# Kernel tuning notes

Measured on AMD Instinct MI355X. Metric: run time of the kernel, lower is better.

Reference implementation:

```python
import jax, jax.numpy as jnp
import numpy as np

B, S, DIM, H, KVH = 2, 1024, 4096, 32, 8
HD = DIM // H          # 128
NREP = H // KVH        # 4
KVD = KVH * HD         # 1024
EPS = 1e-8


def setup_inputs() -> dict:
    key = jax.random.key(0)
    ks = jax.random.split(key, 6)
    x = jax.random.normal(ks[0], (B, S, DIM), jnp.float32)
    wq = jax.random.normal(ks[1], (DIM, DIM), jnp.float32) * 0.02
    wk = jax.random.normal(ks[2], (KVD, DIM), jnp.float32) * 0.02
    wv = jax.random.normal(ks[3], (KVD, DIM), jnp.float32) * 0.02
    wo = jax.random.normal(ks[4], (DIM, DIM), jnp.float32) * 0.02
    scale = jnp.ones((DIM,), jnp.float32)  # RMSNorm scale
    # freq_cis has shape (S, 1) complex so it broadcasts onto both the
    # (B,S,DIM/2) and (B,S,KVD/2) complex views (RoPE applied pre-head-split).
    theta = jnp.arange(S, dtype=jnp.float32)[:, None] * 0.01  # (S,1)
    freqs_cos = jnp.cos(theta)
    freqs_sin = jnp.sin(theta)
    return dict(x=x, scale=scale, wq=wq, wk=wk, wv=wv, wo=wo,
                freqs_cos=freqs_cos, freqs_sin=freqs_sin)


def _rope(t, cos, sin):
    # t: (B,S,D) viewed as (B,S,D/2,2) complex pairs; cos/sin: (S,1)
    t2 = t.reshape(*t.shape[:-1], -1, 2)
    t0, t1 = t2[..., 0], t2[..., 1]
    r0 = t0 * cos - t1 * sin
    r1 = t0 * sin + t1 * cos
    return jnp.stack([r0, r1], axis=-1).reshape(t.shape)


def reference(x, scale, wq, wk, wv, wo, freqs_cos, freqs_sin):
    # RMSNorm
    xn = scale * x * jax.lax.rsqrt(jnp.mean(x * x, axis=-1, keepdims=True) + EPS)
    # QKV projections (nn.Linear: y = x @ W^T)
    q = jnp.einsum('bsd,ed->bse', xn, wq)          # (B,S,DIM)
    k = jnp.einsum('bsd,ed->bse', xn, wk)          # (B,S,KVD)
    v = jnp.einsum('bsd,ed->bse', xn, wv)          # (B,S,KVD)
    # RoPE on full projected dims (as in the original, before head split)
    q = _rope(q, freqs_cos, freqs_sin)
    k = _rope(k, freqs_cos, freqs_sin)
    q = q.reshape(B, S, H, HD)
    k = k.reshape(B, S, KVH, HD)
    v = v.reshape(B, S, KVH, HD)
    # start_pos=0: KV-cache write then read of [:, :S] is identity.
    # GQA expansion via torch .repeat => tile along head axis
    k = jnp.tile(k, (1, 1, NREP, 1))               # (B,S,H,HD)
    v = jnp.tile(v, (1, 1, NREP, 1))
    logits = jnp.einsum('bqhd,bkhd->bhqk', q, k) / jnp.sqrt(jnp.float32(HD))
    causal = jnp.triu(jnp.ones((S, S), bool), 1)   # True above diagonal
    logits = jnp.where(causal, -jnp.inf, logits)
    attn = jax.nn.softmax(logits, axis=-1)
    out = jnp.einsum('bhqk,bkhd->bqhd', attn, v).reshape(B, S, DIM)
    # residual from the NORMALIZED x (the original rebinds x = norm(x))
    return xn + jnp.einsum('bsd,ed->bse', out, wo)
```

## Files before the change

kernel.cpp:

```cpp
#include <hip/hip_runtime.h>
#include <math.h>

#define NB    2
#define NS    1024
#define NDIM  4096
#define NH    32
#define NKVH  8
#define NHD   128
#define NKVD  1024
#define NM    (NB*NS)
#define NQKV  (NDIM + 2*NKVD)

typedef __attribute__((ext_vector_type(8))) short bf16x8;
typedef __attribute__((ext_vector_type(4))) float f32x4;

#define AS3(p) ((__attribute__((address_space(3))) void*)(p))
#define AS1(p) ((const __attribute__((address_space(1))) void*)(p))

__device__ __forceinline__ unsigned short f2bf(float f) {
  unsigned u = __builtin_bit_cast(unsigned, f);
  u += 0x7fffu + ((u >> 16) & 1u);
  return (unsigned short)(u >> 16);
}
__device__ __forceinline__ float bf2f(unsigned short h) {
  unsigned u = ((unsigned)h) << 16;
  return __builtin_bit_cast(float, u);
}
__device__ __forceinline__ void split2(float v, unsigned short& h, unsigned short& l) {
  h = f2bf(v);
  l = f2bf(v - bf2f(h));
}
__device__ __forceinline__ void split8(const float* f, bf16x8& h, bf16x8& l) {
#pragma unroll
  for (int i = 0; i < 8; ++i) {
    unsigned short hh, ll;
    split2(f[i], hh, ll);
    h[i] = (short)hh; l[i] = (short)ll;
  }
}

template <int OFMT>
__global__ __launch_bounds__(256) void rmsnorm_k(const float* __restrict__ x,
                                                 const float* __restrict__ scale,
                                                 unsigned short* __restrict__ xnh,
                                                 unsigned short* __restrict__ xnl,
                                                 float* __restrict__ xnf) {
  const int row = blockIdx.x;
  const float4* xr = (const float4*)(x + (size_t)row * NDIM);
  const float4* sc4 = (const float4*)scale;
  const int t = threadIdx.x;
  float4 v[4];
  float ss = 0.f;
#pragma unroll
  for (int i = 0; i < 4; ++i) {
    v[i] = xr[t + 256 * i];
    ss += v[i].x * v[i].x + v[i].y * v[i].y + v[i].z * v[i].z + v[i].w * v[i].w;
  }
#pragma unroll
  for (int m = 32; m >= 1; m >>= 1) ss += __shfl_xor(ss, m, 64);
  __shared__ float red[4];
  if ((t & 63) == 0) red[t >> 6] = ss;
  __syncthreads();
  const float r = rsqrtf((red[0] + red[1] + red[2] + red[3]) * (1.0f / NDIM) + 1e-8f);
#pragma unroll
  for (int i = 0; i < 4; ++i) {
    const float4 s4 = sc4[t + 256 * i];
    float o[4] = {v[i].x * r * s4.x, v[i].y * r * s4.y, v[i].z * r * s4.z, v[i].w * r * s4.w};
    if (OFMT == 0) {
      ushort4 h4, l4;
      split2(o[0], h4.x, l4.x); split2(o[1], h4.y, l4.y);
      split2(o[2], h4.z, l4.z); split2(o[3], h4.w, l4.w);
      *(ushort4*)&xnh[(size_t)row * NDIM + (t + 256 * i) * 4] = h4;
      *(ushort4*)&xnl[(size_t)row * NDIM + (t + 256 * i) * 4] = l4;
    } else {
      *(float4*)&xnf[(size_t)row * NDIM + (t + 256 * i) * 4] =
          make_float4(o[0], o[1], o[2], o[3]);
    }
  }
}

__global__ __launch_bounds__(256) void splitw_k(const float* __restrict__ src,
                                                unsigned short* __restrict__ dh,
                                                unsigned short* __restrict__ dl,
                                                long long count4) {
  const long long stride = (long long)gridDim.x * 256;
  for (long long i = blockIdx.x * 256LL + threadIdx.x; i < count4; i += stride) {
    const float4 v = ((const float4*)src)[i];
    ushort4 h4, l4;
    split2(v.x, h4.x, l4.x); split2(v.y, h4.y, l4.y);
    split2(v.z, h4.z, l4.z); split2(v.w, h4.w, l4.w);
    ((ushort4*)dh)[i] = h4;
    ((ushort4*)dl)[i] = l4;
  }
}

__global__ __launch_bounds__(256) void zerofill_k(float* __restrict__ p, long long n) {
  const long long stride = (long long)gridDim.x * 256;
  for (long long i = blockIdx.x * 256LL + threadIdx.x; i < n; i += stride) p[i] = 0.f;
}

template <int EPI>
__global__ __launch_bounds__(256) void gemm_split_k(
    const unsigned short* __restrict__ Ah, const unsigned short* __restrict__ Al,
    const unsigned short* __restrict__ Bh, const unsigned short* __restrict__ Bl,
    const float* __restrict__ fc, const float* __restrict__ fs,
    const unsigned short* __restrict__ resh, const unsigned short* __restrict__ resl,
    float* __restrict__ C, int ncol0) {
  constexpr int OW = (EPI == 0) ? NQKV : NDIM;
  __shared__ unsigned short lds[4][4096];

  const int t = threadIdx.x;
  const int wave = t >> 6, lane = t & 63;
  const int wr = wave >> 1, wc = wave & 1;
  const int m0 = blockIdx.x * 128;
  const int n0 = blockIdx.y * 128;

  const int srow = t >> 2;
  const int ke = (((t & 3) ^ ((srow >> 1) & 3)) * 8);
  const size_t arow0 = (size_t)(m0 + srow) * NDIM + ke;
  const size_t arow1 = (size_t)(m0 + 64 + srow) * NDIM + ke;
  const size_t brow0 = (size_t)(n0 + srow) * NDIM + ke;
  const size_t brow1 = (size_t)(n0 + 64 + srow) * NDIM + ke;
  const int ldsoff0 = wave * 512;
  const int ldsoff1 = 2048 + wave * 512;

  f32x4 acc[4][4];
#pragma unroll
  for (int i = 0; i < 4; ++i)
#pragma unroll
    for (int j = 0; j < 4; ++j) acc[i][j] = (f32x4){0.f, 0.f, 0.f, 0.f};

  const int fl = lane & 15;
  const int fq = lane >> 4;

  for (int k0 = 0; k0 < NDIM; k0 += 32) {
    __syncthreads();
    __builtin_amdgcn_global_load_lds(AS1(Ah + arow0 + k0), AS3(&lds[0][ldsoff0]), 16, 0, 0);
    __builtin_amdgcn_global_load_lds(AS1(Ah + arow1 + k0), AS3(&lds[0][ldsoff1]), 16, 0, 0);
    __builtin_amdgcn_global_load_lds(AS1(Al + arow0 + k0), AS3(&lds[1][ldsoff0]), 16, 0, 0);
    __builtin_amdgcn_global_load_lds(AS1(Al + arow1 + k0), AS3(&lds[1][ldsoff1]), 16, 0, 0);
    __builtin_amdgcn_global_load_lds(AS1(Bh + brow0 + k0), AS3(&lds[2][ldsoff0]), 16, 0, 0);
    __builtin_amdgcn_global_load_lds(AS1(Bh + brow1 + k0), AS3(&lds[2][ldsoff1]), 16, 0, 0);
    __builtin_amdgcn_global_load_lds(AS1(Bl + brow0 + k0), AS3(&lds[3][ldsoff0]), 16, 0, 0);
    __builtin_amdgcn_global_load_lds(AS1(Bl + brow1 + k0), AS3(&lds[3][ldsoff1]), 16, 0, 0);
    __syncthreads();

    bf16x8 fah[4], fal[4], fbh[4], fbl[4];
#pragma unroll
    for (int m = 0; m < 4; ++m) {
      const int r = wr * 64 + m * 16 + fl;
      const int idx = r * 32 + ((fq ^ ((r >> 1) & 3)) * 8);
      fah[m] = *(const bf16x8*)&lds[0][idx];
      fal[m] = *(const bf16x8*)&lds[1][idx];
    }
#pragma unroll
    for (int n = 0; n < 4; ++n) {
      const int r = wc * 64 + n * 16 + fl;
      const int idx = r * 32 + ((fq ^ ((r >> 1) & 3)) * 8);
      fbh[n] = *(const bf16x8*)&lds[2][idx];
      fbl[n] = *(const bf16x8*)&lds[3][idx];
    }
#pragma unroll
    for (int m = 0; m < 4; ++m)
#pragma unroll
      for (int n = 0; n < 4; ++n) {
        acc[m][n] = __builtin_amdgcn_mfma_f32_16x16x32_bf16(fah[m], fbh[n], acc[m][n], 0, 0, 0);
        acc[m][n] = __builtin_amdgcn_mfma_f32_16x16x32_bf16(fah[m], fbl[n], acc[m][n], 0, 0, 0);
        acc[m][n] = __builtin_amdgcn_mfma_f32_16x16x32_bf16(fal[m], fbh[n], acc[m][n], 0, 0, 0);
      }
  }

  if (EPI == 0) {
    const int nabs0 = ncol0 + n0;
    const bool rope = (nabs0 < NDIM + NKVD);
    const float qs = (nabs0 < NDIM) ? 0.08838834764831845f : 1.0f;
#pragma unroll
    for (int m = 0; m < 4; ++m)
#pragma unroll
      for (int j = 0; j < 4; ++j) {
        const int gm = m0 + wr * 64 + m * 16 + fq * 4 + j;
        const int si = gm & (NS - 1);
        const float c = fc[si], s = fs[si];
#pragma unroll
        for (int n = 0; n < 4; ++n) {
          const int gn = nabs0 + wc * 64 + n * 16 + fl;
          const float val = acc[m][n][j];
          float o;
          if (rope) {
            const float par = __shfl_xor(val, 1, 64);
            o = ((gn & 1) ? (val * c + par * s) : (val * c - par * s)) * qs;
          } else {
            o = val;
          }
          C[(size_t)gm * OW + gn] = o;
        }
      }
  } else {
#pragma unroll
    for (int m = 0; m < 4; ++m)
#pragma unroll
      for (int j = 0; j < 4; ++j) {
        const int gm = m0 + wr * 64 + m * 16 + fq * 4 + j;
#pragma unroll
        for (int n = 0; n < 4; ++n) {
          const int gn = n0 + wc * 64 + n * 16 + fl;
          const size_t ri = (size_t)gm * NDIM + gn;
          C[ri] = acc[m][n][j] + bf2f(resh[ri]) + bf2f(resl[ri]);
        }
      }
  }
}

__global__ __launch_bounds__(256) void attn_mfma_k(const float* __restrict__ qkv,
                                                   unsigned short* __restrict__ aoh,
                                                   unsigned short* __restrict__ aol) {
  const int qt = (NS / 64 - 1) - blockIdx.x;
  const int bh = blockIdx.y;
  const int b = bh >> 5;
  const int h = bh & 31;
  const int kvh = h & 7;
  const int q0 = qt * 64;

  __shared__ __align__(16) char ldsB[40960];

  const int t = threadIdx.x;
  const int w = t >> 6, lane = t & 63;
  const int l15 = lane & 15, lq = lane >> 4;

  bf16x8 qh[4], ql[4];
  {
    const float* qp = qkv + (size_t)(b * NS + q0 + w * 16 + l15) * NQKV + h * NHD;
#pragma unroll
    for (int c = 0; c < 4; ++c) {
      float qa[8];
      const float4 a = *(const float4*)(qp + lq * 8 + 32 * c);
      const float4 b2 = *(const float4*)(qp + lq * 8 + 32 * c + 4);
      qa[0] = a.x; qa[1] = a.y; qa[2] = a.z; qa[3] = a.w;
      qa[4] = b2.x; qa[5] = b2.y; qa[6] = b2.z; qa[7] = b2.w;
      split8(qa, qh[c], ql[c]);
    }
  }

  f32x4 o[8];
#pragma unroll
  for (int dt = 0; dt < 8; ++dt) o[dt] = (f32x4){0.f, 0.f, 0.f, 0.f};
  float m_run[4] = {-INFINITY, -INFINITY, -INFINITY, -INFINITY};
  float l_run[4] = {0.f, 0.f, 0.f, 0.f};

  const int ntiles = 2 * qt + 2;
  for (int jt = 0; jt < ntiles; ++jt) {
    const int kv0 = jt * 32;
    __syncthreads();
    {
      const int r = t >> 3, d0 = (t & 7) * 16;
      const float* kp = qkv + (size_t)(b * NS + kv0 + r) * NQKV + NDIM + kvh * NHD + d0;
      const float* vp = kp + NKVD;
      float kf[16], vf[16];
#pragma unroll
      for (int i = 0; i < 4; ++i) {
        const float4 k4 = *(const float4*)(kp + 4 * i);
        const float4 v4 = *(const float4*)(vp + 4 * i);
        kf[4 * i] = k4.x; kf[4 * i + 1] = k4.y; kf[4 * i + 2] = k4.z; kf[4 * i + 3] = k4.w;
        vf[4 * i] = v4.x; vf[4 * i + 1] = v4.y; vf[4 * i + 2] = v4.z; vf[4 * i + 3] = v4.w;
      }
#pragma unroll
      for (int g = 0; g < 2; ++g) {
        bf16x8 hi, lo;
        split8(kf + 8 * g, hi, lo);
        const int slotp = (((t & 7) * 2 + g) ^ (r & 7));
        *(bf16x8*)(ldsB + r * 256 + slotp * 16) = hi;
        *(bf16x8*)(ldsB + 8192 + r * 256 + slotp * 16) = lo;
      }
#pragma unroll
      for (int c = 0; c < 16; ++c) {
        const int d = d0 + c;
        unsigned short sh, sl;
        split2(vf[c], sh, sl);
        const int by = 16384 + d * 64 + (((r >> 3) ^ (d & 3)) * 16) + (r & 7) * 2;
        *(unsigned short*)(ldsB + by) = sh;
        *(unsigned short*)(ldsB + 8192 + by) = sl;
      }
    }
    __syncthreads();

    f32x4 s0 = (f32x4){0.f, 0.f, 0.f, 0.f}, s1 = (f32x4){0.f, 0.f, 0.f, 0.f};
    {
      const char* kb = ldsB + l15 * 256;
#pragma unroll
      for (int c = 0; c < 4; ++c) {
        const int sa = ((lq + 4 * c) ^ (l15 & 7)) * 16;
        const bf16x8 k0h = *(const bf16x8*)(kb + sa);
        const bf16x8 k0l = *(const bf16x8*)(kb + 8192 + sa);
        const bf16x8 k1h = *(const bf16x8*)(kb + 4096 + sa);
        const bf16x8 k1l = *(const bf16x8*)(kb + 12288 + sa);
        s0 = __builtin_amdgcn_mfma_f32_16x16x32_bf16(qh[c], k0h, s0, 0, 0, 0);
        s0 = __builtin_amdgcn_mfma_f32_16x16x32_bf16(qh[c], k0l, s0, 0, 0, 0);
        s0 = __builtin_amdgcn_mfma_f32_16x16x32_bf16(ql[c], k0h, s0, 0, 0, 0);
        s1 = __builtin_amdgcn_mfma_f32_16x16x32_bf16(qh[c], k1h, s1, 0, 0, 0);
        s1 = __builtin_amdgcn_mfma_f32_16x16x32_bf16(qh[c], k1l, s1, 0, 0, 0);
        s1 = __builtin_amdgcn_mfma_f32_16x16x32_bf16(ql[c], k1h, s1, 0, 0, 0);
      }
    }

    if (jt >= 2 * qt) {
#pragma unroll
      for (int j = 0; j < 4; ++j) {
        const int qg = q0 + w * 16 + lq * 4 + j;
        if (kv0 + l15 > qg) s0[j] = -INFINITY;
        if (kv0 + 16 + l15 > qg) s1[j] = -INFINITY;
      }
    }

    float resc[4];
#pragma unroll
    for (int j = 0; j < 4; ++j) {
      float mx = fmaxf(s0[j], s1[j]);
#pragma unroll
      for (int mm = 1; mm <= 8; mm <<= 1) mx = fmaxf(mx, __shfl_xor(mx, mm, 64));
      const float mn = fmaxf(m_run[j], mx);
      resc[j] = __expf(m_run[j] - mn);
      s0[j] = __expf(s0[j] - mn);
      s1[j] = __expf(s1[j] - mn);
      float ps = s0[j] + s1[j];
#pragma unroll
      for (int mm = 1; mm <= 8; mm <<= 1) ps += __shfl_xor(ps, mm, 64);
      l_run[j] = l_run[j] * resc[j] + ps;
      m_run[j] = mn;
    }
#pragma unroll
    for (int j = 0; j < 4; ++j) {
      const int q = w * 16 + lq * 4 + j;
      const int by0 = 32768 + q * 128 + (((l15 >> 2) ^ (q & 7)) * 16) + (l15 & 3) * 4;
      *(float*)(ldsB + by0) = s0[j];
      const int kv1 = 16 + l15;
      const int by1 = 32768 + q * 128 + (((kv1 >> 2) ^ (q & 7)) * 16) + (kv1 & 3) * 4;
      *(float*)(ldsB + by1) = s1[j];
    }
#pragma unroll
    for (int dt = 0; dt < 8; ++dt)
#pragma unroll
      for (int j = 0; j < 4; ++j) o[dt][j] *= resc[j];
    __syncthreads();

    {
      const int qrow = w * 16 + l15;
      const int byA = 32768 + qrow * 128 + (((2 * lq) ^ (qrow & 7)) * 16);
      const int byB = 32768 + qrow * 128 + (((2 * lq + 1) ^ (qrow & 7)) * 16);
      const float4 pA = *(const float4*)(ldsB + byA);
      const float4 pB = *(const float4*)(ldsB + byB);
      float pf[8] = {pA.x, pA.y, pA.z, pA.w, pB.x, pB.y, pB.z, pB.w};
      bf16x8 pah, pal;
      split8(pf, pah, pal);
#pragma unroll
      for (int dt = 0; dt < 8; ++dt) {
        const int vrow = dt * 16 + l15;
        const int bv = 16384 + vrow * 64 + ((lq ^ (vrow & 3)) * 16);
        const bf16x8 vbh = *(const bf16x8*)(ldsB + bv);
        const bf16x8 vbl = *(const bf16x8*)(ldsB + bv + 8192);
        o[dt] = __builtin_amdgcn_mfma_f32_16x16x32_bf16(pah, vbh, o[dt], 0, 0, 0);
        o[dt] = __builtin_amdgcn_mfma_f32_16x16x32_bf16(pah, vbl, o[dt], 0, 0, 0);
        o[dt] = __builtin_amdgcn_mfma_f32_16x16x32_bf16(pal, vbh, o[dt], 0, 0, 0);
      }
    }
  }

  float invl[4];
#pragma unroll
  for (int j = 0; j < 4; ++j) invl[j] = 1.0f / l_run[j];
#pragma unroll
  for (int j = 0; j < 4; ++j) {
    const size_t row = (size_t)(b * NS + q0 + w * 16 + lq * 4 + j) * NDIM + h * NHD;
#pragma unroll
    for (int dt = 0; dt < 8; ++dt) {
      unsigned short hh, ll;
      split2(o[dt][j] * invl[j], hh, ll);
      aoh[row + dt * 16 + l15] = hh;
      aol[row + dt * 16 + l15] = ll;
    }
  }
}

#define FBM 64
#define FBK 32
#define LPAD 68

template <int EPI>
__global__ __launch_bounds__(256) void gemm_f32_k(const float* __restrict__ A,
                                                  const float* __restrict__ Wq,
                                                  const float* __restrict__ Wk,
                                                  const float* __restrict__ Wv,
                                                  const float* __restrict__ fc,
                                                  const float* __restrict__ fs,
                                                  const float* __restrict__ resid,
                                                  float* __restrict__ C) {
  __shared__ float As[FBK][LPAD];
  __shared__ float Bs[FBK][LPAD];
  const int t = threadIdx.x;
  const int tx = t & 15, ty = t >> 4;
  const int m0 = blockIdx.y * FBM;
  const int n0 = blockIdx.x * FBM;

  const float* W;
  int wn0;
  if (EPI == 0) {
    if (n0 < NDIM)              { W = Wq; wn0 = n0; }
    else if (n0 < NDIM + NKVD)  { W = Wk; wn0 = n0 - NDIM; }
    else                        { W = Wv; wn0 = n0 - NDIM - NKVD; }
  } else {
    W = Wq; wn0 = n0;
  }

  const int srow = t >> 3;
  const int skk  = (t & 7) * 4;
  const float* Ar = A + (size_t)(m0 + srow) * NDIM + skk;
  const float* Br = W + (size_t)(wn0 + srow) * NDIM + skk;

  float acc[4][4] = {};

  for (int k0 = 0; k0 < NDIM; k0 += FBK) {
    const float4 a0 = *(const float4*)(Ar + k0);
    const float4 a1 = *(const float4*)(Ar + k0 + (size_t)32 * NDIM);
    const float4 b0 = *(const float4*)(Br + k0);
    const float4 b1 = *(const float4*)(Br + k0 + (size_t)32 * NDIM);
    __syncthreads();
    As[skk + 0][srow] = a0.x; As[skk + 1][srow] = a0.y;
    As[skk + 2][srow] = a0.z; As[skk + 3][srow] = a0.w;
    As[skk + 0][srow + 32] = a1.x; As[skk + 1][srow + 32] = a1.y;
    As[skk + 2][srow + 32] = a1.z; As[skk + 3][srow + 32] = a1.w;
    Bs[skk + 0][srow] = b0.x; Bs[skk + 1][srow] = b0.y;
    Bs[skk + 2][srow] = b0.z; Bs[skk + 3][srow] = b0.w;
    Bs[skk + 0][srow + 32] = b1.x; Bs[skk + 1][srow + 32] = b1.y;
    Bs[skk + 2][srow + 32] = b1.z; Bs[skk + 3][srow + 32] = b1.w;
    __syncthreads();
#pragma unroll
    for (int k = 0; k < FBK; ++k) {
      const float4 a = *(const float4*)&As[k][ty * 4];
      const float4 b = *(const float4*)&Bs[k][tx * 4];
      const float av[4] = {a.x, a.y, a.z, a.w};
      const float bv[4] = {b.x, b.y, b.z, b.w};
#pragma unroll
      for (int i = 0; i < 4; ++i)
#pragma unroll
        for (int j = 0; j < 4; ++j)
          acc[i][j] = fmaf(av[i], bv[j], acc[i][j]);
    }
  }

  if (EPI == 0) {
    const bool rope = (n0 < NDIM + NKVD);
    const float qs = (n0 < NDIM) ? 0.08838834764831845f : 1.0f;
#pragma unroll
    for (int i = 0; i < 4; ++i) {
      const int m = m0 + ty * 4 + i;
      const int s = m & (NS - 1);
      const float c = fc[s], sn = fs[s];
      float4 o;
      if (rope) {
        o.x = (acc[i][0] * c - acc[i][1] * sn) * qs;
        o.y = (acc[i][0] * sn + acc[i][1] * c) * qs;
        o.z = (acc[i][2] * c - acc[i][3] * sn) * qs;
        o.w = (acc[i][2] * sn + acc[i][3] * c) * qs;
      } else {
        o = make_float4(acc[i][0], acc[i][1], acc[i][2], acc[i][3]);
      }
      *(float4*)(C + (size_t)m * NQKV + n0 + tx * 4) = o;
    }
  } else {
#pragma unroll
    for (int i = 0; i < 4; ++i) {
      const int m = m0 + ty * 4 + i;
      const float4 r4 = *(const float4*)(resid + (size_t)m * NDIM + n0 + tx * 4);
      *(float4*)(C + (size_t)m * NDIM + n0 + tx * 4) =
          make_float4(acc[i][0] + r4.x, acc[i][1] + r4.y, acc[i][2] + r4.z, acc[i][3] + r4.w);
    }
  }
}

#define BQ 32
#define BKV 32
#define KPAD 132

__global__ __launch_bounds__(256) void attn_f32_k(const float* __restrict__ qkv,
                                                  float* __restrict__ aof) {
  const int qt = blockIdx.x;
  const int bh = blockIdx.y;
  const int b = bh >> 5;
  const int h = bh & 31;
  const int kvh = h & 7;

  __shared__ float Qs[BQ][KPAD];
  __shared__ float Ks[BKV][KPAD];
  __shared__ float Vs[BKV][KPAD];
  __shared__ float Ps[BQ][BKV + 1];

  const int t = threadIdx.x;
  const int lane8 = t & 7;
  const int qi = t >> 3;
  const int q0 = qt * BQ;

  {
    const float* qrow = qkv + (size_t)(b * NS + q0 + qi) * NQKV + h * NHD + lane8 * 16;
#pragma unroll
    for (int i = 0; i < 4; ++i)
      *(float4*)&Qs[qi][lane8 * 16 + 4 * i] = *(const float4*)(qrow + 4 * i);
  }

  float m_run = -INFINITY, l_run = 0.f;
  float4 o0 = {0,0,0,0}, o1 = {0,0,0,0}, o2 = {0,0,0,0}, o3 = {0,0,0,0};

  const size_t kbase = (size_t)(b * NS) * NQKV + NDIM + (size_t)kvh * NHD;
  const size_t vbase = kbase + NKVD;

  for (int jt = 0; jt <= qt; ++jt) {
    const int kv0 = jt * BKV;
    const float* kr = qkv + kbase + (size_t)(kv0 + qi) * NQKV + lane8 * 16;
    const float* vr = qkv + vbase + (size_t)(kv0 + qi) * NQKV + lane8 * 16;
    __syncthreads();
#pragma unroll
    for (int i = 0; i < 4; ++i) {
      *(float4*)&Ks[qi][lane8 * 16 + 4 * i] = *(const float4*)(kr + 4 * i);
      *(float4*)&Vs[qi][lane8 * 16 + 4 * i] = *(const float4*)(vr + 4 * i);
    }
    __syncthreads();

    float scv[4] = {0.f, 0.f, 0.f, 0.f};
#pragma unroll
    for (int d4 = 0; d4 < NHD / 4; ++d4) {
      const float4 q4 = *(const float4*)&Qs[qi][4 * d4];
#pragma unroll
      for (int j = 0; j < 4; ++j) {
        const float4 k4 = *(const float4*)&Ks[lane8 + 8 * j][4 * d4];
        scv[j] = fmaf(q4.x, k4.x, fmaf(q4.y, k4.y, fmaf(q4.z, k4.z, fmaf(q4.w, k4.w, scv[j]))));
      }
    }
    if (jt == qt) {
#pragma unroll
      for (int j = 0; j < 4; ++j)
        if (lane8 + 8 * j > qi) scv[j] = -INFINITY;
    }

    float mloc = fmaxf(fmaxf(scv[0], scv[1]), fmaxf(scv[2], scv[3]));
#pragma unroll
    for (int mm = 1; mm <= 4; mm <<= 1) mloc = fmaxf(mloc, __shfl_xor(mloc, mm, 64));
    const float m_new = fmaxf(m_run, mloc);
    const float resc = __expf(m_run - m_new);
    float p[4], psum = 0.f;
#pragma unroll
    for (int j = 0; j < 4; ++j) { p[j] = __expf(scv[j] - m_new); psum += p[j]; }
#pragma unroll
    for (int mm = 1; mm <= 4; mm <<= 1) psum += __shfl_xor(psum, mm, 64);
    l_run = l_run * resc + psum;
    m_run = m_new;
    o0.x *= resc; o0.y *= resc; o0.z *= resc; o0.w *= resc;
    o1.x *= resc; o1.y *= resc; o1.z *= resc; o1.w *= resc;
    o2.x *= resc; o2.y *= resc; o2.z *= resc; o2.w *= resc;
    o3.x *= resc; o3.y *= resc; o3.z *= resc; o3.w *= resc;
#pragma unroll
    for (int j = 0; j < 4; ++j) Ps[qi][lane8 + 8 * j] = p[j];
    __syncthreads();

#pragma unroll
    for (int kk = 0; kk < BKV; ++kk) {
      const float pv = Ps[qi][kk];
      const float4 v0 = *(const float4*)&Vs[kk][lane8 * 4];
      const float4 v1 = *(const float4*)&Vs[kk][lane8 * 4 + 32];
      const float4 v2 = *(const float4*)&Vs[kk][lane8 * 4 + 64];
      const float4 v3 = *(const float4*)&Vs[kk][lane8 * 4 + 96];
      o0.x = fmaf(pv, v0.x, o0.x); o0.y = fmaf(pv, v0.y, o0.y);
      o0.z = fmaf(pv, v0.z, o0.z); o0.w = fmaf(pv, v0.w, o0.w);
      o1.x = fmaf(pv, v1.x, o1.x); o1.y = fmaf(pv, v1.y, o1.y);
      o1.z = fmaf(pv, v1.z, o1.z); o1.w = fmaf(pv, v1.w, o1.w);
      o2.x = fmaf(pv, v2.x, o2.x); o2.y = fmaf(pv, v2.y, o2.y);
      o2.z = fmaf(pv, v2.z, o2.z); o2.w = fmaf(pv, v2.w, o2.w);
      o3.x = fmaf(pv, v3.x, o3.x); o3.y = fmaf(pv, v3.y, o3.y);
      o3.z = fmaf(pv, v3.z, o3.z); o3.w = fmaf(pv, v3.w, o3.w);
    }
  }

  const float inv_l = 1.0f / l_run;
  const size_t rowb = (size_t)(b * NS + q0 + qi) * NDIM + h * NHD;
  *(float4*)&aof[rowb + lane8 * 4]      = make_float4(o0.x*inv_l, o0.y*inv_l, o0.z*inv_l, o0.w*inv_l);
  *(float4*)&aof[rowb + lane8 * 4 + 32] = make_float4(o1.x*inv_l, o1.y*inv_l, o1.z*inv_l, o1.w*inv_l);
  *(float4*)&aof[rowb + lane8 * 4 + 64] = make_float4(o2.x*inv_l, o2.y*inv_l, o2.z*inv_l, o2.w*inv_l);
  *(float4*)&aof[rowb + lane8 * 4 + 96] = make_float4(o3.x*inv_l, o3.y*inv_l, o3.z*inv_l, o3.w*inv_l);
}

extern "C" void kernel_launch(void* const* d_in, const int* in_sizes, int n_in,
                              void* d_out, int out_size, void* d_ws, size_t ws_size,
                              hipStream_t stream) {
  const float* x  = (const float*)d_in[0];
  const float* sc = (const float*)d_in[1];
  const float* wq = (const float*)d_in[2];
  const float* wk = (const float*)d_in[3];
  const float* wv = (const float*)d_in[4];
  const float* wo = (const float*)d_in[5];
  const float* fc = (const float*)d_in[6];
  const float* fs = (const float*)d_in[7];
  float* out = (float*)d_out;

  const size_t bf = (size_t)NM * NDIM * 2;
  const size_t qkvB = (size_t)NM * NQKV * 4;
  const size_t needA = 4 * bf + qkvB + (size_t)NQKV * NDIM * 4;
  const size_t needB = 4 * bf + qkvB + (size_t)NDIM * NDIM * 4;
  const size_t needC = 2 * (size_t)NM * NDIM * 4 + qkvB;

  if (ws_size >= needB) {
    unsigned short* xnh = (unsigned short*)d_ws;
    unsigned short* xnl = xnh + (size_t)NM * NDIM;
    float* qkv = (float*)(xnl + (size_t)NM * NDIM);
    unsigned short* aoh = (unsigned short*)(qkv + (size_t)NM * NQKV);
    unsigned short* aol = aoh + (size_t)NM * NDIM;
    unsigned short* wh  = aol + (size_t)NM * NDIM;

    rmsnorm_k<0><<<NM, 256, 0, stream>>>(x, sc, xnh, xnl, nullptr);

    if (ws_size >= needA) {
      unsigned short* wl = wh + (size_t)NQKV * NDIM;
      splitw_k<<<1024, 256, 0, stream>>>(wq, wh, wl, (long long)NDIM * NDIM / 4);
      splitw_k<<<1024, 256, 0, stream>>>(wk, wh + (size_t)NDIM * NDIM,
                                         wl + (size_t)NDIM * NDIM, (long long)NKVD * NDIM / 4);
      splitw_k<<<1024, 256, 0, stream>>>(wv, wh + (size_t)(NDIM + NKVD) * NDIM,
                                         wl + (size_t)(NDIM + NKVD) * NDIM,
                                         (long long)NKVD * NDIM / 4);
      gemm_split_k<0><<<dim3(NM / 128, NQKV / 128), 256, 0, stream>>>(
          xnh, xnl, wh, wl, fc, fs, nullptr, nullptr, qkv, 0);
      attn_mfma_k<<<dim3(NS / 64, NB * NH), 256, 0, stream>>>(qkv, aoh, aol);
      splitw_k<<<1024, 256, 0, stream>>>(wo, wh, wl, (long long)NDIM * NDIM / 4);
      gemm_split_k<1><<<dim3(NM / 128, NDIM / 128), 256, 0, stream>>>(
          aoh, aol, wh, wl, nullptr, nullptr, xnh, xnl, out, 0);
    } else {
      unsigned short* wl = wh + (size_t)NDIM * NDIM;
      splitw_k<<<1024, 256, 0, stream>>>(wq, wh, wl, (long long)NDIM * NDIM / 4);
      gemm_split_k<0><<<dim3(NM / 128, NDIM / 128), 256, 0, stream>>>(
          xnh, xnl, wh, wl, fc, fs, nullptr, nullptr, qkv, 0);
      splitw_k<<<1024, 256, 0, stream>>>(wk, wh, wl, (long long)NKVD * NDIM / 4);
      splitw_k<<<1024, 256, 0, stream>>>(wv, wh + (size_t)NKVD * NDIM,
                                         wl + (size_t)NKVD * NDIM, (long long)NKVD * NDIM / 4);
      gemm_split_k<0><<<dim3(NM / 128, (2 * NKVD) / 128), 256, 0, stream>>>(
          xnh, xnl, wh, wl, fc, fs, nullptr, nullptr, qkv, NDIM);
      attn_mfma_k<<<dim3(NS / 64, NB * NH), 256, 0, stream>>>(qkv, aoh, aol);
      splitw_k<<<1024, 256, 0, stream>>>(wo, wh, wl, (long long)NDIM * NDIM / 4);
      gemm_split_k<1><<<dim3(NM / 128, NDIM / 128), 256, 0, stream>>>(
          aoh, aol, wh, wl, nullptr, nullptr, xnh, xnl, out, 0);
    }
  } else if (ws_size >= needC) {
    float* xn   = (float*)d_ws;
    float* qkv  = xn + (size_t)NM * NDIM;
    float* aout = qkv + (size_t)NM * NQKV;

    rmsnorm_k<1><<<NM, 256, 0, stream>>>(x, sc, nullptr, nullptr, xn);
    gemm_f32_k<0><<<dim3(NQKV / FBM, NM / FBM), 256, 0, stream>>>(
        xn, wq, wk, wv, fc, fs, nullptr, qkv);
    attn_f32_k<<<dim3(NS / BQ, NB * NH), 256, 0, stream>>>(qkv, aout);
    gemm_f32_k<1><<<dim3(NDIM / FBM, NM / FBM), 256, 0, stream>>>(
        aout, wo, nullptr, nullptr, nullptr, nullptr, xn, out);
  } else {
    zerofill_k<<<2048, 256, 0, stream>>>(out, (long long)out_size);
  }
}
```

Measured before the change: 1.060 ms.

## Emit split-bf16 Q/K and transposed V from QKV GEMM; async-load into attention

The QKV GEMM epilogue now writes RoPE'd Q and K directly as hi/lo bf16 pairs, and writes V transposed as hi/lo bf16. It no longer stores an fp32 qkv buffer. The attention kernel then loads pre-split, pre-laid-out K and V^T tiles straight into LDS with global_load_lds, instead of loading fp32, splitting and doing a scattered transpose in registers. This halves the intermediate traffic and removes the per-tile conversion work, at the cost of strided transposed V stores in the GEMM epilogue and a changed V swizzle.

```diff
diff --git a/kernel.cpp b/kernel.cpp
--- a/kernel.cpp
+++ b/kernel.cpp
@@ -105,8 +105,11 @@
     const unsigned short* __restrict__ Bh, const unsigned short* __restrict__ Bl,
     const float* __restrict__ fc, const float* __restrict__ fs,
     const unsigned short* __restrict__ resh, const unsigned short* __restrict__ resl,
-    float* __restrict__ C, int ncol0) {
-  constexpr int OW = (EPI == 0) ? NQKV : NDIM;
+    float* __restrict__ C,
+    unsigned short* __restrict__ Qh, unsigned short* __restrict__ Ql,
+    unsigned short* __restrict__ Kh, unsigned short* __restrict__ Kl,
+    unsigned short* __restrict__ VTh, unsigned short* __restrict__ VTl,
+    int ncol0) {
   __shared__ unsigned short lds[4][4096];
 
   const int t = threadIdx.x;
@@ -172,29 +175,49 @@
 
   if (EPI == 0) {
     const int nabs0 = ncol0 + n0;
-    const bool rope = (nabs0 < NDIM + NKVD);
-    const float qs = (nabs0 < NDIM) ? 0.08838834764831845f : 1.0f;
-#pragma unroll
-    for (int m = 0; m < 4; ++m)
-#pragma unroll
-      for (int j = 0; j < 4; ++j) {
-        const int gm = m0 + wr * 64 + m * 16 + fq * 4 + j;
-        const int si = gm & (NS - 1);
-        const float c = fc[si], s = fs[si];
+    if (nabs0 < NDIM + NKVD) {
+      const bool isq = (nabs0 < NDIM);
+      const float qs = isq ? 0.08838834764831845f : 1.0f;
+      unsigned short* dsth = isq ? Qh : Kh;
+      unsigned short* dstl = isq ? Ql : Kl;
+      const int colbase = isq ? nabs0 : (nabs0 - NDIM);
+      const int ow = isq ? NDIM : NKVD;
+#pragma unroll
+      for (int m = 0; m < 4; ++m)
+#pragma unroll
+        for (int j = 0; j < 4; ++j) {
+          const int gm = m0 + wr * 64 + m * 16 + fq * 4 + j;
+          const int si = gm & (NS - 1);
+          const float c = fc[si], s = fs[si];
+#pragma unroll
+          for (int n = 0; n < 4; ++n) {
+            const int gn = colbase + wc * 64 + n * 16 + fl;
+            const float val = acc[m][n][j];
+            const float par = __shfl_xor(val, 1, 64);
+            const float o = ((fl & 1) ? (val * c + par * s) : (val * c - par * s)) * qs;
+            unsigned short hh, ll;
+            split2(o, hh, ll);
+            dsth[(size_t)gm * ow + gn] = hh;
+            dstl[(size_t)gm * ow + gn] = ll;
+          }
+        }
+    } else {
+#pragma unroll
+      for (int m = 0; m < 4; ++m) {
+        const int gmb = m0 + wr * 64 + m * 16 + fq * 4;
 #pragma unroll
         for (int n = 0; n < 4; ++n) {
-          const int gn = nabs0 + wc * 64 + n * 16 + fl;
-          const float val = acc[m][n][j];
-          float o;
-          if (rope) {
-            const float par = __shfl_xor(val, 1, 64);
-            o = ((gn & 1) ? (val * c + par * s) : (val * c - par * s)) * qs;
-          } else {
-            o = val;
-          }
-          C[(size_t)gm * OW + gn] = o;
+          const int f = (nabs0 - NDIM - NKVD) + wc * 64 + n * 16 + fl;
+          ushort4 h4, l4;
+          split2(acc[m][n][0], h4.x, l4.x);
+          split2(acc[m][n][1], h4.y, l4.y);
+          split2(acc[m][n][2], h4.z, l4.z);
+          split2(acc[m][n][3], h4.w, l4.w);
+          *(ushort4*)&VTh[(size_t)f * NM + gmb] = h4;
+          *(ushort4*)&VTl[(size_t)f * NM + gmb] = l4;
         }
       }
+    }
   } else {
 #pragma unroll
     for (int m = 0; m < 4; ++m)
@@ -211,9 +234,11 @@
   }
 }
 
-__global__ __launch_bounds__(256) void attn_mfma_k(const float* __restrict__ qkv,
-                                                   unsigned short* __restrict__ aoh,
-                                                   unsigned short* __restrict__ aol) {
+__global__ __launch_bounds__(256) void attn_mfma2_k(
+    const unsigned short* __restrict__ Qh, const unsigned short* __restrict__ Ql,
+    const unsigned short* __restrict__ Kh, const unsigned short* __restrict__ Kl,
+    const unsigned short* __restrict__ VTh, const unsigned short* __restrict__ VTl,
+    unsigned short* __restrict__ aoh, unsigned short* __restrict__ aol) {
   const int qt = (NS / 64 - 1) - blockIdx.x;
   const int bh = blockIdx.y;
   const int b = bh >> 5;
@@ -229,17 +254,21 @@
 
   bf16x8 qh[4], ql[4];
   {
-    const float* qp = qkv + (size_t)(b * NS + q0 + w * 16 + l15) * NQKV + h * NHD;
+    const size_t qb = (size_t)(b * NS + q0 + w * 16 + l15) * NDIM + h * NHD;
 #pragma unroll
     for (int c = 0; c < 4; ++c) {
-      float qa[8];
-      const float4 a = *(const float4*)(qp + lq * 8 + 32 * c);
-      const float4 b2 = *(const float4*)(qp + lq * 8 + 32 * c + 4);
-      qa[0] = a.x; qa[1] = a.y; qa[2] = a.z; qa[3] = a.w;
-      qa[4] = b2.x; qa[5] = b2.y; qa[6] = b2.z; qa[7] = b2.w;
-      split8(qa, qh[c], ql[c]);
-    }
-  }
+      qh[c] = *(const bf16x8*)&Qh[qb + c * 32 + lq * 8];
+      ql[c] = *(const bf16x8*)&Ql[qb + c * 32 + lq * 8];
+    }
+  }
+
+  const int kr = t >> 4;
+  const int kds = (((t & 15) ^ (kr & 7)) * 8);
+  const size_t kgoff = (size_t)(b * NS + kr) * NKVD + kvh * NHD + kds;
+  const int vd = t >> 2;
+  const int vks = (((t & 3) ^ ((vd >> 1) & 3)) * 8);
+  const size_t vgoff = (size_t)(kvh * NHD + vd) * NM + b * NS + vks;
+  char* const kdst = ldsB + w * 1024;
 
   f32x4 o[8];
 #pragma unroll
@@ -251,48 +280,28 @@
   for (int jt = 0; jt < ntiles; ++jt) {
     const int kv0 = jt * 32;
     __syncthreads();
-    {
-      const int r = t >> 3, d0 = (t & 7) * 16;
-      const float* kp = qkv + (size_t)(b * NS + kv0 + r) * NQKV + NDIM + kvh * NHD + d0;
-      const float* vp = kp + NKVD;
-      float kf[16], vf[16];
-#pragma unroll
-      for (int i = 0; i < 4; ++i) {
-        const float4 k4 = *(const float4*)(kp + 4 * i);
-        const float4 v4 = *(const float4*)(vp + 4 * i);
-        kf[4 * i] = k4.x; kf[4 * i + 1] = k4.y; kf[4 * i + 2] = k4.z; kf[4 * i + 3] = k4.w;
-        vf[4 * i] = v4.x; vf[4 * i + 1] = v4.y; vf[4 * i + 2] = v4.z; vf[4 * i + 3] = v4.w;
-      }
-#pragma unroll
-      for (int g = 0; g < 2; ++g) {
-        bf16x8 hi, lo;
-        split8(kf + 8 * g, hi, lo);
-        const int slotp = (((t & 7) * 2 + g) ^ (r & 7));
-        *(bf16x8*)(ldsB + r * 256 + slotp * 16) = hi;
-        *(bf16x8*)(ldsB + 8192 + r * 256 + slotp * 16) = lo;
-      }
-#pragma unroll
-      for (int c = 0; c < 16; ++c) {
-        const int d = d0 + c;
-        unsigned short sh, sl;
-        split2(vf[c], sh, sl);
-        const int by = 16384 + d * 64 + (((r >> 3) ^ (d & 3)) * 16) + (r & 7) * 2;
-        *(unsigned short*)(ldsB + by) = sh;
-        *(unsigned short*)(ldsB + 8192 + by) = sl;
-      }
+#pragma unroll
+    for (int i = 0; i < 2; ++i) {
+      const size_t kg = kgoff + (size_t)(kv0 + i * 16) * NKVD;
+      const size_t vg = vgoff + kv0 + (size_t)i * 64 * NM;
+      __builtin_amdgcn_global_load_lds(AS1(Kh + kg),  AS3(kdst + i * 4096), 16, 0, 0);
+      __builtin_amdgcn_global_load_lds(AS1(Kl + kg),  AS3(kdst + 8192 + i * 4096), 16, 0, 0);
+      __builtin_amdgcn_global_load_lds(AS1(VTh + vg), AS3(kdst + 16384 + i * 4096), 16, 0, 0);
+      __builtin_amdgcn_global_load_lds(AS1(VTl + vg), AS3(kdst + 24576 + i * 4096), 16, 0, 0);
     }
     __syncthreads();
 
     f32x4 s0 = (f32x4){0.f, 0.f, 0.f, 0.f}, s1 = (f32x4){0.f, 0.f, 0.f, 0.f};
     {
-      const char* kb = ldsB + l15 * 256;
+      const char* kb0 = ldsB + l15 * 256;
+      const char* kb1 = ldsB + (16 + l15) * 256;
 #pragma unroll
       for (int c = 0; c < 4; ++c) {
-        const int sa = ((lq + 4 * c) ^ (l15 & 7)) * 16;
-        const bf16x8 k0h = *(const bf16x8*)(kb + sa);
-        const bf16x8 k0l = *(const bf16x8*)(kb + 8192 + sa);
-        const bf16x8 k1h = *(const bf16x8*)(kb + 4096 + sa);
-        const bf16x8 k1l = *(const bf16x8*)(kb + 12288 + sa);
+        const int sa = (((lq + 4 * c) ^ (l15 & 7)) * 16);
+        const bf16x8 k0h = *(const bf16x8*)(kb0 + sa);
+        const bf16x8 k0l = *(const bf16x8*)(kb0 + 8192 + sa);
+        const bf16x8 k1h = *(const bf16x8*)(kb1 + sa);
+        const bf16x8 k1l = *(const bf16x8*)(kb1 + 8192 + sa);
         s0 = __builtin_amdgcn_mfma_f32_16x16x32_bf16(qh[c], k0h, s0, 0, 0, 0);
         s0 = __builtin_amdgcn_mfma_f32_16x16x32_bf16(qh[c], k0l, s0, 0, 0, 0);
         s0 = __builtin_amdgcn_mfma_f32_16x16x32_bf16(ql[c], k0h, s0, 0, 0, 0);
@@ -354,7 +363,7 @@
 #pragma unroll
       for (int dt = 0; dt < 8; ++dt) {
         const int vrow = dt * 16 + l15;
-        const int bv = 16384 + vrow * 64 + ((lq ^ (vrow & 3)) * 16);
+        const int bv = 16384 + vrow * 64 + ((lq ^ ((vrow >> 1) & 3)) * 16);
         const bf16x8 vbh = *(const bf16x8*)(ldsB + bv);
         const bf16x8 vbl = *(const bf16x8*)(ldsB + bv + 8192);
         o[dt] = __builtin_amdgcn_mfma_f32_16x16x32_bf16(pah, vbh, o[dt], 0, 0, 0);
@@ -598,19 +607,25 @@
   const float* fs = (const float*)d_in[7];
   float* out = (float*)d_out;
 
-  const size_t bf = (size_t)NM * NDIM * 2;
+  const size_t bfp = (size_t)NM * NDIM;
+  const size_t kvp = (size_t)NM * NKVD;
   const size_t qkvB = (size_t)NM * NQKV * 4;
-  const size_t needA = 4 * bf + qkvB + (size_t)NQKV * NDIM * 4;
-  const size_t needB = 4 * bf + qkvB + (size_t)NDIM * NDIM * 4;
-  const size_t needC = 2 * (size_t)NM * NDIM * 4 + qkvB;
+  const size_t needA = (size_t)(4 * bfp) * 2 + qkvB + (size_t)NQKV * NDIM * 4;
+  const size_t needB = (size_t)(4 * bfp) * 2 + qkvB + (size_t)NDIM * NDIM * 4;
+  const size_t needC = 2 * bfp * 4 + qkvB;
 
   if (ws_size >= needB) {
     unsigned short* xnh = (unsigned short*)d_ws;
-    unsigned short* xnl = xnh + (size_t)NM * NDIM;
-    float* qkv = (float*)(xnl + (size_t)NM * NDIM);
-    unsigned short* aoh = (unsigned short*)(qkv + (size_t)NM * NQKV);
-    unsigned short* aol = aoh + (size_t)NM * NDIM;
-    unsigned short* wh  = aol + (size_t)NM * NDIM;
+    unsigned short* xnl = xnh + bfp;
+    unsigned short* qh  = xnl + bfp;
+    unsigned short* ql  = qh + bfp;
+    unsigned short* kh  = ql + bfp;
+    unsigned short* kl  = kh + kvp;
+    unsigned short* vth = kl + kvp;
+    unsigned short* vtl = vth + kvp;
+    unsigned short* aoh = vtl + kvp;
+    unsigned short* aol = aoh + bfp;
+    unsigned short* wh  = aol + bfp;
 
     rmsnorm_k<0><<<NM, 256, 0, stream>>>(x, sc, xnh, xnl, nullptr);
 
@@ -623,29 +638,36 @@
                                          wl + (size_t)(NDIM + NKVD) * NDIM,
                                          (long long)NKVD * NDIM / 4);
       gemm_split_k<0><<<dim3(NM / 128, NQKV / 128), 256, 0, stream>>>(
-          xnh, xnl, wh, wl, fc, fs, nullptr, nullptr, qkv, 0);
-      attn_mfma_k<<<dim3(NS / 64, NB * NH), 256, 0, stream>>>(qkv, aoh, aol);
+          xnh, xnl, wh, wl, fc, fs, nullptr, nullptr, nullptr,
+          qh, ql, kh, kl, vth, vtl, 0);
+      attn_mfma2_k<<<dim3(NS / 64, NB * NH), 256, 0, stream>>>(
+          qh, ql, kh, kl, vth, vtl, aoh, aol);
       splitw_k<<<1024, 256, 0, stream>>>(wo, wh, wl, (long long)NDIM * NDIM / 4);
       gemm_split_k<1><<<dim3(NM / 128, NDIM / 128), 256, 0, stream>>>(
-          aoh, aol, wh, wl, nullptr, nullptr, xnh, xnl, out, 0);
+          aoh, aol, wh, wl, nullptr, nullptr, xnh, xnl, out,
+          nullptr, nullptr, nullptr, nullptr, nullptr, nullptr, 0);
     } else {
       unsigned short* wl = wh + (size_t)NDIM * NDIM;
       splitw_k<<<1024, 256, 0, stream>>>(wq, wh, wl, (long long)NDIM * NDIM / 4);
       gemm_split_k<0><<<dim3(NM / 128, NDIM / 128), 256, 0, stream>>>(
-          xnh, xnl, wh, wl, fc, fs, nullptr, nullptr, qkv, 0);
+          xnh, xnl, wh, wl, fc, fs, nullptr, nullptr, nullptr,
+          qh, ql, kh, kl, vth, vtl, 0);
       splitw_k<<<1024, 256, 0, stream>>>(wk, wh, wl, (long long)NKVD * NDIM / 4);
       splitw_k<<<1024, 256, 0, stream>>>(wv, wh + (size_t)NKVD * NDIM,
                                          wl + (size_t)NKVD * NDIM, (long long)NKVD * NDIM / 4);
       gemm_split_k<0><<<dim3(NM / 128, (2 * NKVD) / 128), 256, 0, stream>>>(
-          xnh, xnl, wh, wl, fc, fs, nullptr, nullptr, qkv, NDIM);
-      attn_mfma_k<<<dim3(NS / 64, NB * NH), 256, 0, stream>>>(qkv, aoh, aol);
+          xnh, xnl, wh, wl, fc, fs, nullptr, nullptr, nullptr,
+          qh, ql, kh, kl, vth, vtl, NDIM);
+      attn_mfma2_k<<<dim3(NS / 64, NB * NH), 256, 0, stream>>>(
+          qh, ql, kh, kl, vth, vtl, aoh, aol);
       splitw_k<<<1024, 256, 0, stream>>>(wo, wh, wl, (long long)NDIM * NDIM / 4);
       gemm_split_k<1><<<dim3(NM / 128, NDIM / 128), 256, 0, stream>>>(
-          aoh, aol, wh, wl, nullptr, nullptr, xnh, xnl, out, 0);
+          aoh, aol, wh, wl, nullptr, nullptr, xnh, xnl, out,
+          nullptr, nullptr, nullptr, nullptr, nullptr, nullptr, 0);
     }
   } else if (ws_size >= needC) {
     float* xn   = (float*)d_ws;
-    float* qkv  = xn + (size_t)NM * NDIM;
+    float* qkv  = xn + bfp;
     float* aout = qkv + (size_t)NM * NQKV;
 
     rmsnorm_k<1><<<NM, 256, 0, stream>>>(x, sc, nullptr, nullptr, xn);
```

Measured after the change: 941.1 us. 1.13x faster.
